# Kernel optimization log

Measured on AMD Instinct MI355X. Metric: run time of the kernel, lower is better.

## Reference

```python
import jax, jax.numpy as jnp
import numpy as np

BUCKETS = 32
DIM = 1024
HEADS = 16
TEMP = 0.75
SINK_ITERS = 7
LOG_EPS = 1e-6
GUMBEL_EPS = 1e-4


def _sinkhorn(r, n_iters):
    # iterative row/col log-normalization, then exp (matches torch loop)
    for _ in range(n_iters):
        r = r - jax.scipy.special.logsumexp(r, axis=2, keepdims=True)
        r = r - jax.scipy.special.logsumexp(r, axis=1, keepdims=True)
    return jnp.exp(r)


def setup_inputs() -> dict:
    key = jax.random.key(0)
    kq, kk, kv, kw, kg = jax.random.split(key, 5)
    B, H, T, DH = 4, 16, 4096, 64
    q = jax.random.normal(kq, (B, H, T, DH), jnp.float32)
    k = jax.random.normal(kk, (B, H, T, DH), jnp.float32)
    v = jax.random.normal(kv, (B, H, T, DH), jnp.float32)
    sort_w = jax.random.normal(kw, (1, H, DH, BUCKETS), jnp.float32)
    u = jax.random.uniform(kg, (B * H, BUCKETS, BUCKETS), jnp.float32, 0.0, 1.0)
    gumbel_noise = -jnp.log(-jnp.log(u + GUMBEL_EPS) + GUMBEL_EPS)
    return {"q": q, "k": k, "v": v, "sort_w": sort_w, "gumbel_noise": gumbel_noise}


def reference(q, k, v, sort_w, gumbel_noise):
    b, h, t, dh = q.shape
    bh = b * h
    bsz = t // BUCKETS  # tokens per bucket
    # bucket: (bh, buckets, bsz, dh)
    qb = q.reshape(bh, BUCKETS, bsz, dh)
    kb = k.reshape(bh, BUCKETS, bsz, dh)
    vb = v.reshape(bh, BUCKETS, bsz, dh)
    # bucket summaries for routing
    b_k_r = kb.sum(axis=2)  # (bh, buckets, dh)
    e_w = jnp.broadcast_to(sort_w, (b, h, dh, BUCKETS)).reshape(bh, dh, BUCKETS)
    R = jnp.log(jax.nn.relu(jnp.einsum('bud,bdv->buv', b_k_r, e_w)) + LOG_EPS)
    R = (R + gumbel_noise) / TEMP
    R = _sinkhorn(R, SINK_ITERS)  # soft permutation matrix (bh, buckets, buckets)
    R = jnp.tril(R, -1)  # causal: only attend to strictly earlier buckets
    # soft-permute key/value buckets
    k_re = jnp.einsum('buv,bvtd->butd', R, kb)
    v_re = jnp.einsum('buv,bvtd->butd', R, vb)
    bk = jnp.concatenate([k_re, kb], axis=2)  # (bh, buckets, 2*bsz, dh)
    bv = jnp.concatenate([v_re, vb], axis=2)
    dots = jnp.einsum('buie,buje->buij', qb, bk) * (DIM ** -0.5)
    attn = jax.nn.softmax(dots, axis=-1)
    out = jnp.einsum('buij,buje->buie', attn, bv)  # (bh, buckets, bsz, dh)
    return out.reshape(b, h, t, dh)
```

## Files before the change

kernel.cpp:

```cpp
#include <hip/hip_runtime.h>
#include <hip/hip_bf16.h>

#define BUCKETS 32
#define BSZ 128
#define DH 64
#define TEMPINV 1.3333333333333333f
#define SINK_ITERS 7
#define LOG_EPS 1e-6f
#define SCALE 0.03125f

typedef short bf16x8 __attribute__((ext_vector_type(8)));
typedef float f32x4 __attribute__((ext_vector_type(4)));

__device__ __forceinline__ void bf8_to_f32(const uint4 x, float* f) {
    f[0] = __uint_as_float(x.x << 16);
    f[1] = __uint_as_float(x.x & 0xffff0000u);
    f[2] = __uint_as_float(x.y << 16);
    f[3] = __uint_as_float(x.y & 0xffff0000u);
    f[4] = __uint_as_float(x.z << 16);
    f[5] = __uint_as_float(x.z & 0xffff0000u);
    f[6] = __uint_as_float(x.w << 16);
    f[7] = __uint_as_float(x.w & 0xffff0000u);
}

__device__ __forceinline__ unsigned f2bf(float f) {
    unsigned x = __float_as_uint(f);
    return (x + 0x7fffu + ((x >> 16) & 1u)) >> 16;
}

__device__ __forceinline__ uint4 packbf8(const float* f) {
    uint4 r;
    r.x = f2bf(f[0]) | (f2bf(f[1]) << 16);
    r.y = f2bf(f[2]) | (f2bf(f[3]) << 16);
    r.z = f2bf(f[4]) | (f2bf(f[5]) << 16);
    r.w = f2bf(f[6]) | (f2bf(f[7]) << 16);
    return r;
}

__device__ __forceinline__ void load_lds16(const uint4* g, uint4* l) {
    __builtin_amdgcn_global_load_lds(
        (const __attribute__((address_space(1))) unsigned int*)g,
        (__attribute__((address_space(3))) unsigned int*)l, 16, 0, 0);
}

__global__ __launch_bounds__(1024) void sink_fused(
    const float* __restrict__ kptr,
    const float* __restrict__ swptr,
    const float* __restrict__ gptr,
    float* __restrict__ Rout)
{
    const int b = blockIdx.x;
    const int h = b & 15;
    const int tid = threadIdx.x;

    __shared__ float bk[BUCKETS][DH];
    __shared__ float swl[DH][BUCKETS];
    __shared__ float R[BUCKETS][BUCKETS + 1];

    {
        const int u = tid >> 5, dp = tid & 31;
        const float2* base = (const float2*)kptr + ((size_t)b * 32 + u) * 4096 + dp;
        float sx = 0.f, sy = 0.f;
        for (int t = 0; t < BSZ; ++t) {
            const float2 a = base[t * 32];
            sx += a.x; sy += a.y;
        }
        bk[u][dp * 2] = sx;
        bk[u][dp * 2 + 1] = sy;
    }
    for (int o = tid; o < DH * BUCKETS; o += 1024)
        swl[o >> 5][o & 31] = swptr[h * DH * BUCKETS + o];
    __syncthreads();

    {
        const int uu = tid >> 5, vv = tid & 31;
        float dot = 0.f;
        for (int d = 0; d < DH; ++d) dot = fmaf(bk[uu][d], swl[d][vv], dot);
        R[uu][vv] = (logf(fmaxf(dot, 0.f) + LOG_EPS) + gptr[b * 1024 + tid]) * TEMPINV;
    }
    __syncthreads();

    const int rr = tid >> 3, sub = tid & 7;
    for (int it = 0; it < SINK_ITERS; ++it) {
        if (tid < 256) {
            float vals[4];
            float m = -1e30f, s = 0.f;
            #pragma unroll
            for (int q = 0; q < 4; ++q) { vals[q] = R[rr][sub * 4 + q]; m = fmaxf(m, vals[q]); }
            m = fmaxf(m, __shfl_xor(m, 1)); m = fmaxf(m, __shfl_xor(m, 2)); m = fmaxf(m, __shfl_xor(m, 4));
            #pragma unroll
            for (int q = 0; q < 4; ++q) s += expf(vals[q] - m);
            s += __shfl_xor(s, 1); s += __shfl_xor(s, 2); s += __shfl_xor(s, 4);
            const float lse = m + logf(s);
            #pragma unroll
            for (int q = 0; q < 4; ++q) R[rr][sub * 4 + q] = vals[q] - lse;
        }
        __syncthreads();
        if (tid < 256) {
            float vals[4];
            float m = -1e30f, s = 0.f;
            #pragma unroll
            for (int q = 0; q < 4; ++q) { vals[q] = R[sub * 4 + q][rr]; m = fmaxf(m, vals[q]); }
            m = fmaxf(m, __shfl_xor(m, 1)); m = fmaxf(m, __shfl_xor(m, 2)); m = fmaxf(m, __shfl_xor(m, 4));
            #pragma unroll
            for (int q = 0; q < 4; ++q) s += expf(vals[q] - m);
            s += __shfl_xor(s, 1); s += __shfl_xor(s, 2); s += __shfl_xor(s, 4);
            const float lse = m + logf(s);
            #pragma unroll
            for (int q = 0; q < 4; ++q) R[sub * 4 + q][rr] = vals[q] - lse;
        }
        __syncthreads();
    }

    {
        const int uu = tid >> 5, vv = tid & 31;
        Rout[b * 1024 + tid] = (vv < uu) ? expf(R[uu][vv]) : 0.f;
    }
}

__global__ __launch_bounds__(256, 4) void reshuffle5_kernel(
    const float* __restrict__ kptr,
    const float* __restrict__ vptr,
    const float* __restrict__ Rmat,
    uint4* __restrict__ kimg,
    uint4* __restrict__ vimg)
{
    const int j0 = blockIdx.x;
    const int b  = blockIdx.y;
    const int tid = threadIdx.x;
    const int w = tid >> 6, g = (tid >> 3) & 7, c8 = tid & 7;
    const int u = g * 4 + w;

    __shared__ float ls[32][4][64];
    __shared__ float lr[32][33];

    for (int o = tid; o < 1024; o += 256)
        lr[o >> 5][o & 31] = Rmat[b * 1024 + o];

    float4* ls4 = (float4*)ls;
    uint4* kdst = kimg + ((size_t)b * 32 + u) * 2048;

    #pragma unroll
    for (int q = 0; q < 2; ++q) {
        const float4* kb4 = (const float4*)kptr + (size_t)b * 65536 + (j0 * 8 + q * 4) * 16;
        for (int it = 0; it < 8; ++it) {
            const int idx = it * 256 + tid;
            const int v = idx >> 6, i = idx & 63;
            ls4[v * 64 + i] = kb4[v * 2048 + i];
        }
        __syncthreads();
        float ka[4][8];
        #pragma unroll
        for (int r = 0; r < 4; ++r)
            #pragma unroll
            for (int t = 0; t < 8; ++t) ka[r][t] = 0.f;
        for (int vv = 0; vv < u; ++vv) {
            const float rwt = lr[u][vv];
            #pragma unroll
            for (int r = 0; r < 4; ++r)
                #pragma unroll
                for (int t = 0; t < 8; ++t)
                    ka[r][t] = fmaf(rwt, ls[vv][r][c8 * 8 + t], ka[r][t]);
        }
        #pragma unroll
        for (int r = 0; r < 4; ++r) {
            const int j = j0 * 8 + q * 4 + r;
            kdst[j * 8 + (c8 ^ (j & 7))] = packbf8(ka[r]);
            float o8[8];
            #pragma unroll
            for (int t = 0; t < 8; ++t) o8[t] = ls[u][r][c8 * 8 + t];
            kdst[(128 + j) * 8 + (c8 ^ (j & 7))] = packbf8(o8);
        }
        __syncthreads();
    }

    unsigned rex[8], rey[8], rez[8], rew[8];
    unsigned orx[8], ory[8], orz[8], orw[8];
    #pragma unroll
    for (int q = 0; q < 2; ++q) {
        const float4* vb4 = (const float4*)vptr + (size_t)b * 65536 + (j0 * 8 + q * 4) * 16;
        for (int it = 0; it < 8; ++it) {
            const int idx = it * 256 + tid;
            const int v = idx >> 6, i = idx & 63;
            ls4[v * 64 + i] = vb4[v * 2048 + i];
        }
        __syncthreads();
        float va[4][8];
        #pragma unroll
        for (int r = 0; r < 4; ++r)
            #pragma unroll
            for (int t = 0; t < 8; ++t) va[r][t] = 0.f;
        for (int vv = 0; vv < u; ++vv) {
            const float rwt = lr[u][vv];
            #pragma unroll
            for (int r = 0; r < 4; ++r)
                #pragma unroll
                for (int t = 0; t < 8; ++t)
                    va[r][t] = fmaf(rwt, ls[vv][r][c8 * 8 + t], va[r][t]);
        }
        if (q == 0) {
            #pragma unroll
            for (int t = 0; t < 8; ++t) {
                rex[t] = f2bf(va[0][t]) | (f2bf(va[1][t]) << 16);
                rey[t] = f2bf(va[2][t]) | (f2bf(va[3][t]) << 16);
                orx[t] = f2bf(ls[u][0][c8 * 8 + t]) | (f2bf(ls[u][1][c8 * 8 + t]) << 16);
                ory[t] = f2bf(ls[u][2][c8 * 8 + t]) | (f2bf(ls[u][3][c8 * 8 + t]) << 16);
            }
        } else {
            #pragma unroll
            for (int t = 0; t < 8; ++t) {
                rez[t] = f2bf(va[0][t]) | (f2bf(va[1][t]) << 16);
                rew[t] = f2bf(va[2][t]) | (f2bf(va[3][t]) << 16);
                orz[t] = f2bf(ls[u][0][c8 * 8 + t]) | (f2bf(ls[u][1][c8 * 8 + t]) << 16);
                orw[t] = f2bf(ls[u][2][c8 * 8 + t]) | (f2bf(ls[u][3][c8 * 8 + t]) << 16);
            }
        }
        __syncthreads();
    }
    {
        uint4* vdst = vimg + ((size_t)b * 32 + u) * 2048;
        #pragma unroll
        for (int t = 0; t < 8; ++t) {
            const int blk = c8 * 8 + (t ^ c8);
            uint4 wre; wre.x = rex[t]; wre.y = rey[t]; wre.z = rez[t]; wre.w = rew[t];
            vdst[j0 * 64 + blk] = wre;
            uint4 wor; wor.x = orx[t]; wor.y = ory[t]; wor.z = orz[t]; wor.w = orw[t];
            vdst[(16 + j0) * 64 + blk] = wor;
        }
    }
}

__global__ __launch_bounds__(128) void attn_fallback(
    const float* __restrict__ qptr,
    const float* __restrict__ kptr,
    const float* __restrict__ vptr,
    const float* __restrict__ Rmat,
    float4* __restrict__ optr)
{
    const int u = blockIdx.x;
    const int b = blockIdx.y;
    const int tid = threadIdx.x;

    __shared__ uint4 sbk[2048];
    __shared__ uint4 sbv[2048];

    const float4* k4 = (const float4*)kptr + (size_t)b * 65536;
    const float4* v4 = (const float4*)vptr + (size_t)b * 65536;
    const float4* q4 = (const float4*)qptr + (size_t)b * 65536;

    const float* Rrow = Rmat + (b * BUCKETS + u) * BUCKETS;
    for (int o = tid; o < 1024; o += 128) {
        float ka[8] = {0.f,0.f,0.f,0.f,0.f,0.f,0.f,0.f};
        float va[8] = {0.f,0.f,0.f,0.f,0.f,0.f,0.f,0.f};
        for (int vv = 0; vv < u; ++vv) {
            const float r = Rrow[vv];
            float4 a = k4[vv * 2048 + 2 * o], c = k4[vv * 2048 + 2 * o + 1];
            ka[0] = fmaf(r, a.x, ka[0]); ka[1] = fmaf(r, a.y, ka[1]);
            ka[2] = fmaf(r, a.z, ka[2]); ka[3] = fmaf(r, a.w, ka[3]);
            ka[4] = fmaf(r, c.x, ka[4]); ka[5] = fmaf(r, c.y, ka[5]);
            ka[6] = fmaf(r, c.z, ka[6]); ka[7] = fmaf(r, c.w, ka[7]);
            float4 av = v4[vv * 2048 + 2 * o], cv = v4[vv * 2048 + 2 * o + 1];
            va[0] = fmaf(r, av.x, va[0]); va[1] = fmaf(r, av.y, va[1]);
            va[2] = fmaf(r, av.z, va[2]); va[3] = fmaf(r, av.w, va[3]);
            va[4] = fmaf(r, cv.x, va[4]); va[5] = fmaf(r, cv.y, va[5]);
            va[6] = fmaf(r, cv.z, va[6]); va[7] = fmaf(r, cv.w, va[7]);
        }
        sbk[o] = packbf8(ka);
        sbv[o] = packbf8(va);
        float4 a = k4[u * 2048 + 2 * o], c = k4[u * 2048 + 2 * o + 1];
        float f[8] = {a.x,a.y,a.z,a.w,c.x,c.y,c.z,c.w};
        sbk[1024 + o] = packbf8(f);
        float4 av = v4[u * 2048 + 2 * o], cv = v4[u * 2048 + 2 * o + 1];
        float gg[8] = {av.x,av.y,av.z,av.w,cv.x,cv.y,cv.z,cv.w};
        sbv[1024 + o] = packbf8(gg);
    }
    __syncthreads();

    const int i = tid;
    float qr[64];
    const float4* qrow = q4 + (u * 128 + i) * 16;
    for (int d4 = 0; d4 < 16; ++d4) {
        float4 t = qrow[d4];
        qr[d4 * 4 + 0] = t.x; qr[d4 * 4 + 1] = t.y;
        qr[d4 * 4 + 2] = t.z; qr[d4 * 4 + 3] = t.w;
    }

    float acc[64];
    for (int d = 0; d < 64; ++d) acc[d] = 0.f;
    float l = 0.f;

    for (int j = 0; j < 256; ++j) {
        float s = 0.f;
        for (int d8 = 0; d8 < 8; ++d8) {
            float f[8];
            bf8_to_f32(sbk[j * 8 + d8], f);
            for (int t = 0; t < 8; ++t) s = fmaf(qr[d8 * 8 + t], f[t], s);
        }
        const float p = __expf(s * SCALE);
        l += p;
        for (int d8 = 0; d8 < 8; ++d8) {
            float f[8];
            bf8_to_f32(sbv[j * 8 + d8], f);
            for (int t = 0; t < 8; ++t)
                acc[d8 * 8 + t] = fmaf(p, f[t], acc[d8 * 8 + t]);
        }
    }

    const float inv = 1.f / l;
    float4* orow = optr + (size_t)b * 65536 + (u * 128 + i) * 16;
    for (int d4 = 0; d4 < 16; ++d4) {
        float4 t;
        t.x = acc[d4 * 4 + 0] * inv;
        t.y = acc[d4 * 4 + 1] * inv;
        t.z = acc[d4 * 4 + 2] * inv;
        t.w = acc[d4 * 4 + 3] * inv;
        orow[d4] = t;
    }
}

__global__ __launch_bounds__(256) void attn_mfma2(
    const float* __restrict__ qptr,
    const uint4* __restrict__ kimg,
    const uint4* __restrict__ vimg,
    float* __restrict__ optr)
{
    const int u = blockIdx.x;
    const int b = blockIdx.y;
    const int tid = threadIdx.x;
    const int lane = tid & 63;
    const int w = tid >> 6;
    const int lg = lane >> 4;
    const int lr = lane & 15;

    __shared__ uint4 sK[2048];
    __shared__ uint4 sV[2048];
    __shared__ uint4 sP[1024];

    const size_t tile = (size_t)b * 32 + u;
    const uint4* gk = kimg + tile * 2048;
    const uint4* gv = vimg + tile * 2048;

    #pragma unroll
    for (int it = 0; it < 8; ++it)
        load_lds16(gk + it * 256 + tid, &sK[it * 256 + (w << 6)]);
    #pragma unroll
    for (int it = 0; it < 8; ++it)
        load_lds16(gv + it * 256 + tid, &sV[it * 256 + (w << 6)]);

    const float* qbase = qptr + (size_t)b * 262144 + (size_t)u * 8192;
    bf16x8 qf[2][2];
    #pragma unroll
    for (int mt = 0; mt < 2; ++mt)
        #pragma unroll
        for (int c = 0; c < 2; ++c) {
            const int row = w * 32 + mt * 16 + lr;
            const float4* qr = (const float4*)(qbase + row * 64 + (c * 4 + lg) * 8);
            float4 a = qr[0], cc = qr[1];
            float f[8] = {a.x * SCALE, a.y * SCALE, a.z * SCALE, a.w * SCALE,
                          cc.x * SCALE, cc.y * SCALE, cc.z * SCALE, cc.w * SCALE};
            uint4 tq = packbf8(f);
            qf[mt][c] = *(bf16x8*)&tq;
        }
    __syncthreads();

    uint4* sPw = sP + w * 256;
    unsigned short* sPh = (unsigned short*)sPw;

    f32x4 acc[2][4];
    float lsum[2][4];
    #pragma unroll
    for (int mt = 0; mt < 2; ++mt) {
        #pragma unroll
        for (int nt = 0; nt < 4; ++nt) {
            acc[mt][nt][0] = 0.f; acc[mt][nt][1] = 0.f;
            acc[mt][nt][2] = 0.f; acc[mt][nt][3] = 0.f;
        }
        #pragma unroll
        for (int r = 0; r < 4; ++r) lsum[mt][r] = 0.f;
    }

    for (int kb = 0; kb < 4; ++kb) {
        bf16x8 kf[4][2];
        #pragma unroll
        for (int nt = 0; nt < 4; ++nt)
            #pragma unroll
            for (int c = 0; c < 2; ++c) {
                const int j = kb * 64 + nt * 16 + lr;
                const int dcu = c * 4 + lg;
                uint4 t = sK[j * 8 + (dcu ^ (j & 7))];
                kf[nt][c] = *(bf16x8*)&t;
            }
        f32x4 s[2][4];
        #pragma unroll
        for (int mt = 0; mt < 2; ++mt)
            #pragma unroll
            for (int nt = 0; nt < 4; ++nt) {
                s[mt][nt][0] = 0.f; s[mt][nt][1] = 0.f;
                s[mt][nt][2] = 0.f; s[mt][nt][3] = 0.f;
            }
        __builtin_amdgcn_s_setprio(1);
        #pragma unroll
        for (int c = 0; c < 2; ++c)
            #pragma unroll
            for (int mt = 0; mt < 2; ++mt)
                #pragma unroll
                for (int nt = 0; nt < 4; ++nt)
                    s[mt][nt] = __builtin_amdgcn_mfma_f32_16x16x32_bf16(
                        qf[mt][c], kf[nt][c], s[mt][nt], 0, 0, 0);
        __builtin_amdgcn_s_setprio(0);

        #pragma unroll
        for (int mt = 0; mt < 2; ++mt)
            #pragma unroll
            for (int nt = 0; nt < 4; ++nt)
                #pragma unroll
                for (int r = 0; r < 4; ++r) {
                    const float p = __expf(s[mt][nt][r]);
                    lsum[mt][r] += p;
                    const int row = mt * 16 + lg * 4 + r;
                    const int col = nt * 16 + lr;
                    sPh[row * 64 + (((col >> 3) ^ (row & 7)) << 3) + (col & 7)] =
                        (unsigned short)f2bf(p);
                }
        asm volatile("s_waitcnt lgkmcnt(0)" ::: "memory");
        __builtin_amdgcn_sched_barrier(0);

        bf16x8 pf[2][2];
        #pragma unroll
        for (int mt = 0; mt < 2; ++mt)
            #pragma unroll
            for (int c = 0; c < 2; ++c) {
                const int row = mt * 16 + lr;
                const int dcu = c * 4 + lg;
                uint4 t = sPw[row * 8 + (dcu ^ (row & 7))];
                pf[mt][c] = *(bf16x8*)&t;
            }
        bf16x8 vf[4][2];
        #pragma unroll
        for (int nt = 0; nt < 4; ++nt)
            #pragma unroll
            for (int c = 0; c < 2; ++c) {
                const int p = kb * 8 + c * 4 + lg;
                const int d = nt * 16 + lr;
                const int blk = (d >> 3) * 8 + ((d & 7) ^ ((d >> 3) & 7));
                uint4 t = sV[p * 64 + blk];
                vf[nt][c] = *(bf16x8*)&t;
            }
        __builtin_amdgcn_s_setprio(1);
        #pragma unroll
        for (int c = 0; c < 2; ++c)
            #pragma unroll
            for (int mt = 0; mt < 2; ++mt)
                #pragma unroll
                for (int nt = 0; nt < 4; ++nt)
                    acc[mt][nt] = __builtin_amdgcn_mfma_f32_16x16x32_bf16(
                        pf[mt][c], vf[nt][c], acc[mt][nt], 0, 0, 0);
        __builtin_amdgcn_s_setprio(0);
    }

    #pragma unroll
    for (int mt = 0; mt < 2; ++mt)
        #pragma unroll
        for (int r = 0; r < 4; ++r) {
            float sum = lsum[mt][r];
            sum += __shfl_xor(sum, 1);
            sum += __shfl_xor(sum, 2);
            sum += __shfl_xor(sum, 4);
            sum += __shfl_xor(sum, 8);
            const float inv = 1.f / sum;
            const int row = mt * 16 + lg * 4 + r;
            float* orow = optr + (size_t)b * 262144 +
                          (size_t)(u * 128 + w * 32 + row) * 64;
            #pragma unroll
            for (int nt = 0; nt < 4; ++nt)
                orow[nt * 16 + lr] = acc[mt][nt][r] * inv;
        }
}

extern "C" void kernel_launch(void* const* d_in, const int* in_sizes, int n_in,
                              void* d_out, int out_size, void* d_ws, size_t ws_size,
                              hipStream_t stream) {
    const float* q  = (const float*)d_in[0];
    const float* k  = (const float*)d_in[1];
    const float* v  = (const float*)d_in[2];
    const float* sw = (const float*)d_in[3];
    const float* g  = (const float*)d_in[4];

    float* R    = (float*)d_ws;
    uint4* kimg = (uint4*)((char*)d_ws + 1048576);
    uint4* vimg = (uint4*)((char*)d_ws + 1048576 + 67108864);
    const bool big_ws = (ws_size >= (size_t)1048576 + 2u * 67108864u);

    sink_fused<<<dim3(64), dim3(1024), 0, stream>>>(k, sw, g, R);
    if (big_ws) {
        reshuffle5_kernel<<<dim3(16, 64), dim3(256), 0, stream>>>(k, v, R, kimg, vimg);
        attn_mfma2<<<dim3(32, 64), dim3(256), 0, stream>>>(q, kimg, vimg, (float*)d_out);
    } else {
        attn_fallback<<<dim3(32, 64), dim3(128), 0, stream>>>(q, k, v, R, (float4*)d_out);
    }
}
```

Before: 339.0 us.

## Load full 8-row K/V slabs per pass and stage V image stores through LDS

The reshuffle kernel now loads all eight token rows per bucket in one pass into a doubled 64KB LDS tile, instead of two four-row halves, which halves the number of barriers and load phases. The V output is packed into LDS and then written to global memory with a cooperative loop so stores are coalesced. The min-occupancy hint on launch bounds is dropped. In exchange, each thread holds 64 accumulators and LDS use doubles, which lowers occupancy.

```diff
diff --git a/kernel.cpp b/kernel.cpp
--- a/kernel.cpp
+++ b/kernel.cpp
@@ -118,7 +118,7 @@
     }
 }
 
-__global__ __launch_bounds__(256, 4) void reshuffle5_kernel(
+__global__ __launch_bounds__(256) void reshuffle4_kernel(
     const float* __restrict__ kptr,
     const float* __restrict__ vptr,
     const float* __restrict__ Rmat,
@@ -131,101 +131,101 @@
     const int w = tid >> 6, g = (tid >> 3) & 7, c8 = tid & 7;
     const int u = g * 4 + w;
 
-    __shared__ float ls[32][4][64];
+    __shared__ float ls[32][8][64];
     __shared__ float lr[32][33];
 
     for (int o = tid; o < 1024; o += 256)
         lr[o >> 5][o & 31] = Rmat[b * 1024 + o];
 
     float4* ls4 = (float4*)ls;
-    uint4* kdst = kimg + ((size_t)b * 32 + u) * 2048;
-
-    #pragma unroll
-    for (int q = 0; q < 2; ++q) {
-        const float4* kb4 = (const float4*)kptr + (size_t)b * 65536 + (j0 * 8 + q * 4) * 16;
-        for (int it = 0; it < 8; ++it) {
+
+    {
+        const float4* kb4 = (const float4*)kptr + (size_t)b * 65536 + j0 * 128;
+        for (int it = 0; it < 16; ++it) {
             const int idx = it * 256 + tid;
-            const int v = idx >> 6, i = idx & 63;
-            ls4[v * 64 + i] = kb4[v * 2048 + i];
-        }
-        __syncthreads();
-        float ka[4][8];
-        #pragma unroll
-        for (int r = 0; r < 4; ++r)
+            const int v = idx >> 7, i = idx & 127;
+            ls4[v * 128 + i] = kb4[v * 2048 + i];
+        }
+    }
+    __syncthreads();
+    {
+        float ka[8][8];
+        #pragma unroll
+        for (int r = 0; r < 8; ++r)
             #pragma unroll
             for (int t = 0; t < 8; ++t) ka[r][t] = 0.f;
         for (int vv = 0; vv < u; ++vv) {
             const float rwt = lr[u][vv];
             #pragma unroll
-            for (int r = 0; r < 4; ++r)
+            for (int r = 0; r < 8; ++r)
                 #pragma unroll
                 for (int t = 0; t < 8; ++t)
                     ka[r][t] = fmaf(rwt, ls[vv][r][c8 * 8 + t], ka[r][t]);
         }
-        #pragma unroll
-        for (int r = 0; r < 4; ++r) {
-            const int j = j0 * 8 + q * 4 + r;
-            kdst[j * 8 + (c8 ^ (j & 7))] = packbf8(ka[r]);
+        uint4* kdst = kimg + ((size_t)b * 32 + u) * 2048;
+        #pragma unroll
+        for (int r = 0; r < 8; ++r) {
+            kdst[(j0 * 8 + r) * 8 + (c8 ^ r)] = packbf8(ka[r]);
             float o8[8];
             #pragma unroll
             for (int t = 0; t < 8; ++t) o8[t] = ls[u][r][c8 * 8 + t];
-            kdst[(128 + j) * 8 + (c8 ^ (j & 7))] = packbf8(o8);
-        }
-        __syncthreads();
-    }
-
-    unsigned rex[8], rey[8], rez[8], rew[8];
-    unsigned orx[8], ory[8], orz[8], orw[8];
-    #pragma unroll
-    for (int q = 0; q < 2; ++q) {
-        const float4* vb4 = (const float4*)vptr + (size_t)b * 65536 + (j0 * 8 + q * 4) * 16;
-        for (int it = 0; it < 8; ++it) {
+            kdst[(128 + j0 * 8 + r) * 8 + (c8 ^ r)] = packbf8(o8);
+        }
+    }
+    __syncthreads();
+
+    {
+        const float4* vb4 = (const float4*)vptr + (size_t)b * 65536 + j0 * 128;
+        for (int it = 0; it < 16; ++it) {
             const int idx = it * 256 + tid;
-            const int v = idx >> 6, i = idx & 63;
-            ls4[v * 64 + i] = vb4[v * 2048 + i];
-        }
-        __syncthreads();
-        float va[4][8];
-        #pragma unroll
-        for (int r = 0; r < 4; ++r)
+            const int v = idx >> 7, i = idx & 127;
+            ls4[v * 128 + i] = vb4[v * 2048 + i];
+        }
+    }
+    __syncthreads();
+    {
+        uint4 wor[8];
+        #pragma unroll
+        for (int t = 0; t < 8; ++t) {
+            wor[t].x = f2bf(ls[u][0][c8 * 8 + t]) | (f2bf(ls[u][1][c8 * 8 + t]) << 16);
+            wor[t].y = f2bf(ls[u][2][c8 * 8 + t]) | (f2bf(ls[u][3][c8 * 8 + t]) << 16);
+            wor[t].z = f2bf(ls[u][4][c8 * 8 + t]) | (f2bf(ls[u][5][c8 * 8 + t]) << 16);
+            wor[t].w = f2bf(ls[u][6][c8 * 8 + t]) | (f2bf(ls[u][7][c8 * 8 + t]) << 16);
+        }
+        float va[8][8];
+        #pragma unroll
+        for (int r = 0; r < 8; ++r)
             #pragma unroll
             for (int t = 0; t < 8; ++t) va[r][t] = 0.f;
         for (int vv = 0; vv < u; ++vv) {
             const float rwt = lr[u][vv];
             #pragma unroll
-            for (int r = 0; r < 4; ++r)
+            for (int r = 0; r < 8; ++r)
                 #pragma unroll
                 for (int t = 0; t < 8; ++t)
                     va[r][t] = fmaf(rwt, ls[vv][r][c8 * 8 + t], va[r][t]);
         }
-        if (q == 0) {
-            #pragma unroll
-            for (int t = 0; t < 8; ++t) {
-                rex[t] = f2bf(va[0][t]) | (f2bf(va[1][t]) << 16);
-                rey[t] = f2bf(va[2][t]) | (f2bf(va[3][t]) << 16);
-                orx[t] = f2bf(ls[u][0][c8 * 8 + t]) | (f2bf(ls[u][1][c8 * 8 + t]) << 16);
-                ory[t] = f2bf(ls[u][2][c8 * 8 + t]) | (f2bf(ls[u][3][c8 * 8 + t]) << 16);
-            }
-        } else {
-            #pragma unroll
-            for (int t = 0; t < 8; ++t) {
-                rez[t] = f2bf(va[0][t]) | (f2bf(va[1][t]) << 16);
-                rew[t] = f2bf(va[2][t]) | (f2bf(va[3][t]) << 16);
-                orz[t] = f2bf(ls[u][0][c8 * 8 + t]) | (f2bf(ls[u][1][c8 * 8 + t]) << 16);
-                orw[t] = f2bf(ls[u][2][c8 * 8 + t]) | (f2bf(ls[u][3][c8 * 8 + t]) << 16);
-            }
-        }
         __syncthreads();
-    }
-    {
-        uint4* vdst = vimg + ((size_t)b * 32 + u) * 2048;
+
+        uint4* img = (uint4*)ls;
         #pragma unroll
         for (int t = 0; t < 8; ++t) {
             const int blk = c8 * 8 + (t ^ c8);
-            uint4 wre; wre.x = rex[t]; wre.y = rey[t]; wre.z = rez[t]; wre.w = rew[t];
-            vdst[j0 * 64 + blk] = wre;
-            uint4 wor; wor.x = orx[t]; wor.y = ory[t]; wor.z = orz[t]; wor.w = orw[t];
-            vdst[(16 + j0) * 64 + blk] = wor;
+            uint4 wre;
+            wre.x = f2bf(va[0][t]) | (f2bf(va[1][t]) << 16);
+            wre.y = f2bf(va[2][t]) | (f2bf(va[3][t]) << 16);
+            wre.z = f2bf(va[4][t]) | (f2bf(va[5][t]) << 16);
+            wre.w = f2bf(va[6][t]) | (f2bf(va[7][t]) << 16);
+            img[u * 64 + blk] = wre;
+            img[2048 + u * 64 + blk] = wor[t];
+        }
+        __syncthreads();
+
+        for (int o = tid; o < 2048; o += 256) {
+            const int uu = o >> 6, blk = o & 63;
+            const size_t tb = ((size_t)b * 32 + uu) * 2048;
+            vimg[tb + j0 * 64 + blk] = img[o];
+            vimg[tb + (16 + j0) * 64 + blk] = img[2048 + o];
         }
     }
 }
@@ -493,7 +493,7 @@
 
     sink_fused<<<dim3(64), dim3(1024), 0, stream>>>(k, sw, g, R);
     if (big_ws) {
-        reshuffle5_kernel<<<dim3(16, 64), dim3(256), 0, stream>>>(k, v, R, kimg, vimg);
+        reshuffle4_kernel<<<dim3(16, 64), dim3(256), 0, stream>>>(k, v, R, kimg, vimg);
         attn_mfma2<<<dim3(32, 64), dim3(256), 0, stream>>>(q, kimg, vimg, (float*)d_out);
     } else {
         attn_fallback<<<dim3(32, 64), dim3(128), 0, stream>>>(q, k, v, R, (float4*)d_out);
```

Result: faster. 327.7 us (-3.3%).
